# Optimization experiments

Measured on AMD Instinct MI355X. Metric: run time of the kernel, lower is better.

Reference implementation:

```python
import jax, jax.numpy as jnp
import numpy as np

N_ATOMS = 16384
APC = 64            # atoms per conformer
N_CONF = 256        # 64 mols * 4 confs
N_MOL = 64
DEG = 32
E = N_ATOMS * DEG
H = 128             # hidden_channels = num_filters = out_channels
G = 50              # num_gaussians
L = 6               # num_interactions
CUTOFF = 10.0
LOG2 = float(np.log(2.0))


def ssp(x):
    # ShiftedSoftplus: softplus(x) - log(2)
    return jax.nn.softplus(x) - LOG2


def setup_inputs() -> dict:
    key = jax.random.key(0)
    ks = jax.random.split(key, 24)
    rng = np.random.default_rng(0)

    z = jnp.asarray(rng.integers(1, 100, size=(N_ATOMS,)), dtype=jnp.int64 if jax.config.jax_enable_x64 else jnp.int32)
    # positions uniform in a 5A box -> all intra-conformer distances < cutoff
    pos = jax.random.uniform(ks[0], (N_ATOMS, 3), dtype=jnp.float32) * 5.0

    # within-conformer random edges, no self loops (radius_graph surrogate)
    i = np.repeat(np.arange(N_ATOMS), DEG)
    off = rng.integers(1, APC, size=E)
    j = (i // APC) * APC + (i % APC + off) % APC
    edge_index = jnp.asarray(np.stack([j, i]), dtype=jnp.int32)  # [2,E] (source, target)

    atom_to_conf = jnp.asarray(np.arange(N_ATOMS) // APC, dtype=jnp.int32)
    conf_to_mol = jnp.asarray(np.arange(N_CONF) // (N_CONF // N_MOL), dtype=jnp.int32)

    s = 0.05
    p = {
        'emb':     jax.random.normal(ks[1], (120, H), jnp.float32) * s,
        # per-interaction stacked params [L, ...]
        'mlp_w1':  jax.random.normal(ks[2], (L, G, H), jnp.float32) * s,
        'mlp_b1':  jnp.zeros((L, H), jnp.float32),
        'mlp_w2':  jax.random.normal(ks[3], (L, H, H), jnp.float32) * s,
        'mlp_b2':  jnp.zeros((L, H), jnp.float32),
        'cf_w1':   jax.random.normal(ks[4], (L, H, H), jnp.float32) * s,
        'cf_w2':   jax.random.normal(ks[5], (L, H, H), jnp.float32) * s,
        'cf_b2':   jnp.zeros((L, H), jnp.float32),
        'int_w':   jax.random.normal(ks[6], (L, H, H), jnp.float32) * s,
        'int_b':   jnp.zeros((L, H), jnp.float32),
        # readout head
        'out_w1':  jax.random.normal(ks[7], (H, H), jnp.float32) * s,
        'out_b1':  jnp.zeros((H,), jnp.float32),
        'out_w2':  jax.random.normal(ks[8], (H, H), jnp.float32) * s,
        'out_b2':  jnp.zeros((H,), jnp.float32),
        'head_w1': jax.random.normal(ks[9], (H, H // 2), jnp.float32) * s,
        'head_b1': jnp.zeros((H // 2,), jnp.float32),
        'head_w2': jax.random.normal(ks[10], (H // 2, 1), jnp.float32) * s,
        'head_b2': jnp.zeros((1,), jnp.float32),
    }
    return dict(z=z, pos=pos, edge_index=edge_index, atom_to_conf=atom_to_conf,
                conf_to_mol=conf_to_mol, **p)


def reference(z, pos, edge_index, atom_to_conf, conf_to_mol, emb,
              mlp_w1, mlp_b1, mlp_w2, mlp_b2, cf_w1, cf_w2, cf_b2,
              int_w, int_b, out_w1, out_b1, out_w2, out_b2,
              head_w1, head_b1, head_w2, head_b2):
    row, col = edge_index[0], edge_index[1]  # message from row, aggregated at col

    h = emb[z]                                             # [N,H]
    edge_weight = jnp.linalg.norm(pos[row] - pos[col], axis=-1)  # [E]

    # GaussianSmearing
    offset = jnp.linspace(0.0, CUTOFF, G)
    coeff = -0.5 / (offset[1] - offset[0]) ** 2
    edge_attr = jnp.exp(coeff * (edge_weight[:, None] - offset[None, :]) ** 2)  # [E,G]

    C = 0.5 * (jnp.cos(edge_weight * jnp.pi / CUTOFF) + 1.0)  # cosine cutoff [E]

    for l in range(L):
        # filter network on edge features, modulated by cutoff envelope
        Wf = ssp(edge_attr @ mlp_w1[l] + mlp_b1[l]) @ mlp_w2[l] + mlp_b2[l]
        Wf = Wf * C[:, None]                               # [E,H]
        xf = h @ cf_w1[l]                                  # lin1 (no bias) [N,H]
        msg = xf[row] * Wf                                 # gather * filter [E,H]
        agg = jax.ops.segment_sum(msg, col, num_segments=N_ATOMS)  # scatter-add [N,H]
        xc = agg @ cf_w2[l] + cf_b2[l]                     # lin2
        h = h + (ssp(xc) @ int_w[l] + int_b[l])            # act, lin, residual

    h = ssp(h @ out_w1 + out_b1)
    h = h @ out_w2 + out_b2                                # [N,H]

    conf_emb = jax.ops.segment_sum(h, atom_to_conf, num_segments=N_CONF)   # [C,H]
    mol_emb = jax.ops.segment_sum(conf_emb, conf_to_mol, num_segments=N_MOL)  # [M,H]

    out = (ssp(mol_emb @ head_w1 + head_b1) @ head_w2 + head_b2)[:, 0]  # [M]
    return out
```

## Files before the change

kernel.cpp:

```cpp
#include <hip/hip_runtime.h>
#include <math.h>

#define N_ATOMS 16384
#define APC 64
#define N_CONF 256
#define N_MOL 64
#define DEG 32
#define NEDGE (N_ATOMS * DEG)
#define H 128
#define G 50
#define NL 6
#define TP0 512
#define TPB 4096
#define CUTOFF 10.0f
#define WBLK 160
#define TBLK (NL * 256)

typedef __attribute__((ext_vector_type(8))) short short8_t;
typedef __attribute__((ext_vector_type(4))) float f32x4;
typedef __attribute__((ext_vector_type(2))) float f32x2;

__device__ __forceinline__ float ssp_f(float x) {
  float e = __expf(-fabsf(x));
  return fmaxf(x, 0.f) + __logf(1.f + e) - 0.69314718055994531f;
}
__device__ __forceinline__ unsigned short bf16_rne(float x) {
  unsigned u = __float_as_uint(x);
  unsigned r = u + 0x7FFF + ((u >> 16) & 1);
  return (unsigned short)(r >> 16);
}
__device__ __forceinline__ float bf16_to_f(unsigned short s) {
  return __uint_as_float(((unsigned)s) << 16);
}
__device__ __forceinline__ float bflo(unsigned u) { return __uint_as_float(u << 16); }
__device__ __forceinline__ float bfhi(unsigned u) { return __uint_as_float(u & 0xFFFF0000u); }

__global__ __launch_bounds__(256) void k_setup(
    const float* __restrict__ cf_w1, const float* __restrict__ cf_w2,
    const float* __restrict__ int_w, const float* __restrict__ out_w1,
    const float* __restrict__ out_w2, short* __restrict__ PW,
    const float* __restrict__ w1, const float* __restrict__ b1,
    const float* __restrict__ w2, const float* __restrict__ b2,
    unsigned short* __restrict__ Tb, int* __restrict__ cnt) {
  __shared__ float g2s[2][64];
  __shared__ float S2[2][128];
  __shared__ float OutS[4][132];
  const int b = blockIdx.x;
  const int tid = threadIdx.x;
  if (b == 0 && tid == 0) *cnt = 0;
  if (b < WBLK) {
    int e = b * 256 + tid;
    int g = e >> 11, t = e & 2047;
    int kb = t >> 9, rem = t & 511, nt = rem >> 6, lane = rem & 63;
    int quad = lane >> 4, ln2 = lane & 15;
    int kbase = kb * 32 + quad * 8;
    int n = nt * 16 + ln2;
    const float* src;
    if (g < 12) {
      int l = g >> 1;
      src = (g & 1) ? (int_w + l * 16384) : (cf_w2 + l * 16384);
    } else if (g < 18) {
      src = cf_w1 + (g - 12) * 16384;
    } else {
      src = (g == 18) ? out_w1 : out_w2;
    }
    short hv[8], lv[8];
    #pragma unroll
    for (int j = 0; j < 8; j++) {
      float x = src[(kbase + j) * H + n];
      unsigned short hb = bf16_rne(x);
      hv[j] = (short)hb;
      lv[j] = (short)bf16_rne(x - bf16_to_f(hb));
    }
    size_t base = (size_t)g * 32768 + (size_t)t * 8;
    *(short8_t*)&PW[base] = *(short8_t*)hv;
    *(short8_t*)&PW[base + 16384] = *(short8_t*)lv;
  } else {
    int bb = b - WBLK;
    const int l = bb >> 8, q = bb & 255;
    const int grp = tid >> 7, c = tid & 127;
    const int p_min =
        (int)((float)(q * 16) * ((float)(TP0 - 1) / (float)(TPB - 1)));
    const float gspace = CUTOFF / (float)(G - 1);
    const float coeff = -0.5f / (gspace * gspace);
    const float* W1 = w1 + l * G * H;
    const float* W2 = w2 + l * H * H;
    #pragma unroll 1
    for (int r = 0; r < 2; r++) {
      int pt = r * 2 + grp;
      int p = p_min + pt;
      if (p > TP0 - 1) p = TP0 - 1;
      float d = (float)p * (CUTOFF / (float)(TP0 - 1));
      if (c < G) {
        float x = d - (float)c * gspace;
        g2s[grp][c] = __expf(coeff * x * x);
      }
      __syncthreads();
      float s = b1[l * H + c];
      #pragma unroll 5
      for (int i = 0; i < G; i++) s += g2s[grp][i] * W1[i * H + c];
      S2[grp][c] = ssp_f(s);
      __syncthreads();
      float o = b2[l * H + c];
      #pragma unroll 8
      for (int j = 0; j < H; j++) o += S2[grp][j] * W2[j * H + c];
      float Cc = 0.5f * (__cosf(d * (3.14159265358979f / CUTOFF)) + 1.f);
      OutS[pt][c] = o * Cc;
      __syncthreads();
    }
    int p4o = tid >> 4, cg = tid & 15;
    int p4 = q * 16 + p4o;
    float u = (float)p4 * ((float)(TP0 - 1) / (float)(TPB - 1));
    int i = (int)u;
    if (i > TP0 - 2) i = TP0 - 2;
    float f = u - (float)i;
    int li = i - p_min;
    short8_t ov;
    #pragma unroll
    for (int j = 0; j < 4; j++) {
      float a0 = OutS[li][cg * 4 + j], a1 = OutS[li + 1][cg * 4 + j];
      ov[j] = (short)bf16_rne(a0 + f * (a1 - a0));
      float b0 = OutS[li][64 + cg * 4 + j], b1v = OutS[li + 1][64 + cg * 4 + j];
      ov[4 + j] = (short)bf16_rne(b0 + f * (b1v - b0));
    }
    *(short8_t*)&Tb[((size_t)l * TPB + p4) * H + cg * 8] = ov;
  }
}

#define MFMA(a, b, c) __builtin_amdgcn_mfma_f32_16x16x32_bf16((a), (b), (c), 0, 0, 0)

__device__ __forceinline__ void gemm_1x2(const short (*AH)[136], const short (*AL)[136],
                                         const short* __restrict__ pw,
                                         int rt, int ct2, int lane, int quad, int ln,
                                         f32x4 acc[2]) {
  #pragma unroll
  for (int kb = 0; kb < 4; kb++) {
    int ko = kb * 32 + quad * 8;
    int row = rt * 16 + ln;
    short8_t ah = *(const short8_t*)&AH[row][ko];
    short8_t al = *(const short8_t*)&AL[row][ko];
    #pragma unroll
    for (int ct = 0; ct < 2; ct++) {
      const short* pb = pw + ((size_t)(kb * 8 + ct2 * 2 + ct) * 64 + lane) * 8;
      short8_t bh = *(const short8_t*)pb;
      short8_t bl = *(const short8_t*)(pb + 16384);
      acc[ct] = MFMA(ah, bh, acc[ct]);
      acc[ct] = MFMA(ah, bl, acc[ct]);
      acc[ct] = MFMA(al, bh, acc[ct]);
    }
  }
}

__global__ __launch_bounds__(1024, 1) void k_mega(
    const int* __restrict__ z, const float* __restrict__ emb,
    const float* __restrict__ pos, const int* __restrict__ esrc,
    const unsigned short* __restrict__ Tb,
    const short* __restrict__ PW, const float* __restrict__ cf_b2,
    const float* __restrict__ int_b, const float* __restrict__ out_b1,
    const float* __restrict__ out_b2, float* __restrict__ ce,
    const float* __restrict__ hw1, const float* __restrict__ hb1,
    const float* __restrict__ hw2, const float* __restrict__ hb2,
    int* __restrict__ cnt, float* __restrict__ outp) {
  __shared__ float xs[64][132];
  __shared__ __align__(16) short hH[64][136], hL[64][136];
  __shared__ __align__(16) short tH[64][136], tL[64][136];
  __shared__ __align__(16) short S1H[64][136], S1L[64][136];
  __shared__ int pks[2048];
  __shared__ float ps[4][128];
  __shared__ int is_last;
  const int conf = blockIdx.x;
  const int tid = threadIdx.x;
  const int lane = tid & 63, w = tid >> 6;
  const int quad = lane >> 4, ln = lane & 15;
  const int rt = w & 3, ct2 = w >> 2;
  const int eg = lane >> 4, c0 = (lane & 15) * 4;

  float* posl = &xs[0][0];
  if (tid < 192) posl[tid] = pos[conf * 192 + tid];

  {
    int r = tid >> 4, cb = (tid & 15) * 8;
    const float* src = emb + (size_t)z[conf * 64 + r] * H + cb;
    float4 v0 = *(const float4*)src, v1 = *(const float4*)(src + 4);
    float vv[8] = {v0.x, v0.y, v0.z, v0.w, v1.x, v1.y, v1.z, v1.w};
    short hv[8], lv[8];
    #pragma unroll
    for (int u = 0; u < 8; u++) {
      unsigned short hb = bf16_rne(vv[u]);
      hv[u] = (short)hb;
      lv[u] = (short)bf16_rne(vv[u] - bf16_to_f(hb));
    }
    *(short8_t*)&hH[r][cb] = *(short8_t*)hv;
    *(short8_t*)&hL[r][cb] = *(short8_t*)lv;
  }
  __syncthreads();

  #pragma unroll
  for (int e0 = 0; e0 < 2; e0++) {
    int e = e0 * 1024 + tid;
    int s = esrc[conf * 2048 + e] & (APC - 1);
    int t = e >> 5;
    float dx = posl[s * 3 + 0] - posl[t * 3 + 0];
    float dy = posl[s * 3 + 1] - posl[t * 3 + 1];
    float dz = posl[s * 3 + 2] - posl[t * 3 + 2];
    float d = sqrtf(dx * dx + dy * dy + dz * dz);
    int i = (int)(d * ((float)(TPB - 1) / CUTOFF) + 0.5f);
    if (i > TPB - 1) i = TPB - 1;
    if (i < 0) i = 0;
    pks[e] = (i << 8) | (s << 20);
  }
  __syncthreads();

  {
    f32x4 acc[2] = {{0.f, 0.f, 0.f, 0.f}, {0.f, 0.f, 0.f, 0.f}};
    gemm_1x2(hH, hL, PW + (size_t)12 * 32768, rt, ct2, lane, quad, ln, acc);
    #pragma unroll
    for (int ct = 0; ct < 2; ct++) {
      int col = (ct2 * 2 + ct) * 16 + ln;
      #pragma unroll
      for (int reg = 0; reg < 4; reg++)
        xs[rt * 16 + quad * 4 + reg][col] = acc[ct][reg];
    }
  }
  __syncthreads();

  for (int l = 0; l < NL; l++) {
    const char* Tlb = (const char*)(Tb + (size_t)l * TPB * H) + ln * 16;
    #pragma unroll 1
    for (int aa = 0; aa < 4; aa++) {
      int a2 = w * 4 + aa;
      int ms[8];
      uint4 tvv[8];
      #pragma unroll
      for (int it = 0; it < 8; it++) {
        ms[it] = pks[a2 * DEG + it * 4 + eg];
        tvv[it] = *(const uint4*)(Tlb + (ms[it] & 0xFFFFF));
      }
      f32x2 ac0 = {0.f, 0.f}, ac1 = {0.f, 0.f}, ac2 = {0.f, 0.f}, ac3 = {0.f, 0.f};
      #pragma unroll
      for (int it = 0; it < 8; it++) {
        int sl = ms[it] >> 20;
        const float* xr = &xs[sl][c0];
        float4 x0 = *(const float4*)xr;
        float4 x1 = *(const float4*)(xr + 64);
        uint4 tv = tvv[it];
        ac0 = __builtin_elementwise_fma((f32x2){bflo(tv.x), bfhi(tv.x)},
                                        (f32x2){x0.x, x0.y}, ac0);
        ac1 = __builtin_elementwise_fma((f32x2){bflo(tv.y), bfhi(tv.y)},
                                        (f32x2){x0.z, x0.w}, ac1);
        ac2 = __builtin_elementwise_fma((f32x2){bflo(tv.z), bfhi(tv.z)},
                                        (f32x2){x1.x, x1.y}, ac2);
        ac3 = __builtin_elementwise_fma((f32x2){bflo(tv.w), bfhi(tv.w)},
                                        (f32x2){x1.z, x1.w}, ac3);
      }
      float accs[8] = {ac0.x, ac0.y, ac1.x, ac1.y, ac2.x, ac2.y, ac3.x, ac3.y};
      #pragma unroll
      for (int j = 0; j < 8; j++) {
        accs[j] += __shfl_xor(accs[j], 16);
        accs[j] += __shfl_xor(accs[j], 32);
      }
      float va = eg == 0 ? accs[0] : eg == 1 ? accs[2] : eg == 2 ? accs[4] : accs[6];
      float vb = eg == 0 ? accs[1] : eg == 1 ? accs[3] : eg == 2 ? accs[5] : accs[7];
      unsigned short ha = bf16_rne(va), hb = bf16_rne(vb);
      unsigned short la = bf16_rne(va - bf16_to_f(ha));
      unsigned short lb = bf16_rne(vb - bf16_to_f(hb));
      int cw = (eg >> 1) * 64 + c0 + (eg & 1) * 2;
      *(short2*)&S1H[a2][cw] = make_short2((short)ha, (short)hb);
      *(short2*)&S1L[a2][cw] = make_short2((short)la, (short)lb);
    }
    __syncthreads();
    {
      f32x4 acc[2] = {{0.f, 0.f, 0.f, 0.f}, {0.f, 0.f, 0.f, 0.f}};
      gemm_1x2(S1H, S1L, PW + (size_t)(2 * l) * 32768, rt, ct2, lane, quad, ln, acc);
      #pragma unroll
      for (int ct = 0; ct < 2; ct++) {
        int col = (ct2 * 2 + ct) * 16 + ln;
        float bb = cf_b2[l * H + col];
        #pragma unroll
        for (int reg = 0; reg < 4; reg++) {
          int row = rt * 16 + quad * 4 + reg;
          float v = ssp_f(acc[ct][reg] + bb);
          unsigned short hb = bf16_rne(v);
          tH[row][col] = (short)hb;
          tL[row][col] = (short)bf16_rne(v - bf16_to_f(hb));
        }
      }
    }
    __syncthreads();
    {
      f32x4 acc[2] = {{0.f, 0.f, 0.f, 0.f}, {0.f, 0.f, 0.f, 0.f}};
      gemm_1x2(tH, tL, PW + (size_t)(2 * l + 1) * 32768, rt, ct2, lane, quad, ln, acc);
      #pragma unroll
      for (int ct = 0; ct < 2; ct++) {
        int col = (ct2 * 2 + ct) * 16 + ln;
        float bb = int_b[l * H + col];
        #pragma unroll
        for (int reg = 0; reg < 4; reg++) {
          int row = rt * 16 + quad * 4 + reg;
          float hv = bf16_to_f((unsigned short)hH[row][col]) +
                     bf16_to_f((unsigned short)hL[row][col]);
          float v = acc[ct][reg] + bb + hv;
          unsigned short hb = bf16_rne(v);
          hH[row][col] = (short)hb;
          hL[row][col] = (short)bf16_rne(v - bf16_to_f(hb));
        }
      }
    }
    __syncthreads();
    if (l < NL - 1) {
      f32x4 acc[2] = {{0.f, 0.f, 0.f, 0.f}, {0.f, 0.f, 0.f, 0.f}};
      gemm_1x2(hH, hL, PW + (size_t)(13 + l) * 32768, rt, ct2, lane, quad, ln, acc);
      #pragma unroll
      for (int ct = 0; ct < 2; ct++) {
        int col = (ct2 * 2 + ct) * 16 + ln;
        #pragma unroll
        for (int reg = 0; reg < 4; reg++)
          xs[rt * 16 + quad * 4 + reg][col] = acc[ct][reg];
      }
      __syncthreads();
    }
  }

  {
    f32x4 acc[2] = {{0.f, 0.f, 0.f, 0.f}, {0.f, 0.f, 0.f, 0.f}};
    gemm_1x2(hH, hL, PW + (size_t)18 * 32768, rt, ct2, lane, quad, ln, acc);
    #pragma unroll
    for (int ct = 0; ct < 2; ct++) {
      int col = (ct2 * 2 + ct) * 16 + ln;
      float bb = out_b1[col];
      #pragma unroll
      for (int reg = 0; reg < 4; reg++) {
        int row = rt * 16 + quad * 4 + reg;
        float v = ssp_f(acc[ct][reg] + bb);
        unsigned short hb = bf16_rne(v);
        tH[row][col] = (short)hb;
        tL[row][col] = (short)bf16_rne(v - bf16_to_f(hb));
      }
    }
  }
  __syncthreads();
  {
    f32x4 acc[2] = {{0.f, 0.f, 0.f, 0.f}, {0.f, 0.f, 0.f, 0.f}};
    gemm_1x2(tH, tL, PW + (size_t)19 * 32768, rt, ct2, lane, quad, ln, acc);
    #pragma unroll
    for (int ct = 0; ct < 2; ct++) {
      int col = (ct2 * 2 + ct) * 16 + ln;
      float s = acc[ct][0] + acc[ct][1] + acc[ct][2] + acc[ct][3];
      s += __shfl_xor(s, 16);
      s += __shfl_xor(s, 32);
      if (quad == 0) ps[rt][col] = s;
    }
  }
  __syncthreads();
  if (tid < 128) {
    float v = ps[0][tid] + ps[1][tid] + ps[2][tid] + ps[3][tid] +
              64.f * out_b2[tid];
    __hip_atomic_store(&ce[conf * 128 + tid], v, __ATOMIC_RELAXED,
                       __HIP_MEMORY_SCOPE_AGENT);
  }
  __syncthreads();
  if (tid == 0) {
    __threadfence();
    int old = __hip_atomic_fetch_add(cnt, 1, __ATOMIC_ACQ_REL,
                                     __HIP_MEMORY_SCOPE_AGENT);
    is_last = (old == N_CONF - 1) ? 1 : 0;
  }
  __syncthreads();
  if (is_last) {
    __threadfence();
    float* mol = &xs[0][0];
    for (int t = tid; t < N_MOL * 128; t += 1024) {
      int m = t >> 7, c = t & 127;
      const float* b = ce + (size_t)(m * 4) * 128;
      float s = __hip_atomic_load(&b[c], __ATOMIC_RELAXED, __HIP_MEMORY_SCOPE_AGENT) +
                __hip_atomic_load(&b[128 + c], __ATOMIC_RELAXED, __HIP_MEMORY_SCOPE_AGENT) +
                __hip_atomic_load(&b[256 + c], __ATOMIC_RELAXED, __HIP_MEMORY_SCOPE_AGENT) +
                __hip_atomic_load(&b[384 + c], __ATOMIC_RELAXED, __HIP_MEMORY_SCOPE_AGENT);
      mol[t] = s;
    }
    __syncthreads();
    float* q = (float*)&S1H[0][0];
    for (int t = tid; t < N_MOL * 64; t += 1024) {
      int m = t >> 6, j = t & 63;
      float qq = hb1[j];
      #pragma unroll 8
      for (int c = 0; c < H; c++) qq += mol[m * 128 + c] * hw1[c * 64 + j];
      q[t] = ssp_f(qq);
    }
    __syncthreads();
    if (tid < N_MOL) {
      float o = hb2[0];
      #pragma unroll 8
      for (int j = 0; j < 64; j++) o += q[tid * 64 + j] * hw2[j];
      outp[tid] = o;
    }
  }
}

extern "C" void kernel_launch(void* const* d_in, const int* in_sizes, int n_in,
                              void* d_out, int out_size, void* d_ws, size_t ws_size,
                              hipStream_t stream) {
  const int*   z       = (const int*)d_in[0];
  const float* pos     = (const float*)d_in[1];
  const int*   eidx    = (const int*)d_in[2];
  const float* emb     = (const float*)d_in[5];
  const float* mlp_w1  = (const float*)d_in[6];
  const float* mlp_b1  = (const float*)d_in[7];
  const float* mlp_w2  = (const float*)d_in[8];
  const float* mlp_b2  = (const float*)d_in[9];
  const float* cf_w1   = (const float*)d_in[10];
  const float* cf_w2   = (const float*)d_in[11];
  const float* cf_b2   = (const float*)d_in[12];
  const float* int_w   = (const float*)d_in[13];
  const float* int_b   = (const float*)d_in[14];
  const float* out_w1  = (const float*)d_in[15];
  const float* out_b1  = (const float*)d_in[16];
  const float* out_w2  = (const float*)d_in[17];
  const float* out_b2  = (const float*)d_in[18];
  const float* head_w1 = (const float*)d_in[19];
  const float* head_b1 = (const float*)d_in[20];
  const float* head_w2 = (const float*)d_in[21];
  const float* head_b2 = (const float*)d_in[22];

  char* ws = (char*)d_ws;
  unsigned short* Tb = (unsigned short*)ws;
  short* PW  = (short*)(ws + (size_t)NL * TPB * H * 2);
  float* ce  = (float*)((char*)PW + (size_t)20 * 32768 * 2);
  int*   cnt = (int*)((char*)ce + (size_t)N_CONF * H * 4);

  k_setup<<<WBLK + TBLK, 256, 0, stream>>>(cf_w1, cf_w2, int_w, out_w1, out_w2,
                                           PW, mlp_w1, mlp_b1, mlp_w2, mlp_b2,
                                           Tb, cnt);

  k_mega<<<N_CONF, 1024, 0, stream>>>(z, emb, pos, eidx, Tb, PW, cf_b2, int_b,
                                      out_b1, out_b2, ce,
                                      head_w1, head_b1, head_w2, head_b2,
                                      cnt, (float*)d_out);
}
```

Baseline: 262.9 us.

## Retile warp GEMMs to 32x16 tiles, prefetch gather loads, keep residual in registers

Result: slower. 359.5 us (+36.8%).

```diff
diff --git a/kernel.cpp b/kernel.cpp
--- a/kernel.cpp
+++ b/kernel.cpp
@@ -129,24 +129,28 @@
 
 #define MFMA(a, b, c) __builtin_amdgcn_mfma_f32_16x16x32_bf16((a), (b), (c), 0, 0, 0)
 
-__device__ __forceinline__ void gemm_1x2(const short (*AH)[136], const short (*AL)[136],
+__device__ __forceinline__ void gemm_rt2(const short (*AH)[140], const short (*AL)[140],
                                          const short* __restrict__ pw,
-                                         int rt, int ct2, int lane, int quad, int ln,
+                                         int rt2, int nt, int lane, int quad, int ln,
                                          f32x4 acc[2]) {
+  short8_t bh[4], bl[4];
+  #pragma unroll
+  for (int kb = 0; kb < 4; kb++) {
+    const short* pb = pw + ((size_t)(kb * 8 + nt) * 64 + lane) * 8;
+    bh[kb] = *(const short8_t*)pb;
+    bl[kb] = *(const short8_t*)(pb + 16384);
+  }
   #pragma unroll
   for (int kb = 0; kb < 4; kb++) {
     int ko = kb * 32 + quad * 8;
-    int row = rt * 16 + ln;
-    short8_t ah = *(const short8_t*)&AH[row][ko];
-    short8_t al = *(const short8_t*)&AL[row][ko];
-    #pragma unroll
-    for (int ct = 0; ct < 2; ct++) {
-      const short* pb = pw + ((size_t)(kb * 8 + ct2 * 2 + ct) * 64 + lane) * 8;
-      short8_t bh = *(const short8_t*)pb;
-      short8_t bl = *(const short8_t*)(pb + 16384);
-      acc[ct] = MFMA(ah, bh, acc[ct]);
-      acc[ct] = MFMA(ah, bl, acc[ct]);
-      acc[ct] = MFMA(al, bh, acc[ct]);
+    #pragma unroll
+    for (int rtt = 0; rtt < 2; rtt++) {
+      int row = rt2 * 32 + rtt * 16 + ln;
+      short8_t ah = *(const short8_t*)&AH[row][ko];
+      short8_t al = *(const short8_t*)&AL[row][ko];
+      acc[rtt] = MFMA(ah, bh[kb], acc[rtt]);
+      acc[rtt] = MFMA(ah, bl[kb], acc[rtt]);
+      acc[rtt] = MFMA(al, bh[kb], acc[rtt]);
     }
   }
 }
@@ -162,18 +166,19 @@
     const float* __restrict__ hw2, const float* __restrict__ hb2,
     int* __restrict__ cnt, float* __restrict__ outp) {
   __shared__ float xs[64][132];
-  __shared__ __align__(16) short hH[64][136], hL[64][136];
-  __shared__ __align__(16) short tH[64][136], tL[64][136];
-  __shared__ __align__(16) short S1H[64][136], S1L[64][136];
+  __shared__ __align__(16) short hH[64][140], hL[64][140];
+  __shared__ __align__(16) short tH[64][140], tL[64][140];
+  __shared__ __align__(16) short S1H[64][140], S1L[64][140];
   __shared__ int pks[2048];
-  __shared__ float ps[4][128];
+  __shared__ float ps[2][128];
   __shared__ int is_last;
   const int conf = blockIdx.x;
   const int tid = threadIdx.x;
   const int lane = tid & 63, w = tid >> 6;
   const int quad = lane >> 4, ln = lane & 15;
-  const int rt = w & 3, ct2 = w >> 2;
+  const int rt2 = w & 1, nt = w >> 1;
   const int eg = lane >> 4, c0 = (lane & 15) * 4;
+  const int col = nt * 16 + ln;
 
   float* posl = &xs[0][0];
   if (tid < 192) posl[tid] = pos[conf * 192 + tid];
@@ -194,6 +199,16 @@
     *(short8_t*)&hL[r][cb] = *(short8_t*)lv;
   }
   __syncthreads();
+
+  f32x4 hreg[2];
+  #pragma unroll
+  for (int rtt = 0; rtt < 2; rtt++)
+    #pragma unroll
+    for (int reg = 0; reg < 4; reg++) {
+      int row = rt2 * 32 + rtt * 16 + quad * 4 + reg;
+      hreg[rtt][reg] = bf16_to_f((unsigned short)hH[row][col]) +
+                       bf16_to_f((unsigned short)hL[row][col]);
+    }
 
   #pragma unroll
   for (int e0 = 0; e0 < 2; e0++) {
@@ -213,28 +228,35 @@
 
   {
     f32x4 acc[2] = {{0.f, 0.f, 0.f, 0.f}, {0.f, 0.f, 0.f, 0.f}};
-    gemm_1x2(hH, hL, PW + (size_t)12 * 32768, rt, ct2, lane, quad, ln, acc);
-    #pragma unroll
-    for (int ct = 0; ct < 2; ct++) {
-      int col = (ct2 * 2 + ct) * 16 + ln;
+    gemm_rt2(hH, hL, PW + (size_t)12 * 32768, rt2, nt, lane, quad, ln, acc);
+    #pragma unroll
+    for (int rtt = 0; rtt < 2; rtt++)
       #pragma unroll
       for (int reg = 0; reg < 4; reg++)
-        xs[rt * 16 + quad * 4 + reg][col] = acc[ct][reg];
-    }
+        xs[rt2 * 32 + rtt * 16 + quad * 4 + reg][col] = acc[rtt][reg];
   }
   __syncthreads();
 
   for (int l = 0; l < NL; l++) {
     const char* Tlb = (const char*)(Tb + (size_t)l * TPB * H) + ln * 16;
+    int ms[8];
+    uint4 tvv[8];
+    #pragma unroll
+    for (int it = 0; it < 8; it++) {
+      ms[it] = pks[(w * 4) * DEG + it * 4 + eg];
+      tvv[it] = *(const uint4*)(Tlb + (ms[it] & 0xFFFFF));
+    }
     #pragma unroll 1
     for (int aa = 0; aa < 4; aa++) {
       int a2 = w * 4 + aa;
-      int ms[8];
-      uint4 tvv[8];
-      #pragma unroll
-      for (int it = 0; it < 8; it++) {
-        ms[it] = pks[a2 * DEG + it * 4 + eg];
-        tvv[it] = *(const uint4*)(Tlb + (ms[it] & 0xFFFFF));
+      int msn[8];
+      uint4 tvn[8];
+      if (aa < 3) {
+        #pragma unroll
+        for (int it = 0; it < 8; it++) {
+          msn[it] = pks[(a2 + 1) * DEG + it * 4 + eg];
+          tvn[it] = *(const uint4*)(Tlb + (msn[it] & 0xFFFFF));
+        }
       }
       f32x2 ac0 = {0.f, 0.f}, ac1 = {0.f, 0.f}, ac2 = {0.f, 0.f}, ac3 = {0.f, 0.f};
       #pragma unroll
@@ -267,94 +289,88 @@
       int cw = (eg >> 1) * 64 + c0 + (eg & 1) * 2;
       *(short2*)&S1H[a2][cw] = make_short2((short)ha, (short)hb);
       *(short2*)&S1L[a2][cw] = make_short2((short)la, (short)lb);
+      if (aa < 3) {
+        #pragma unroll
+        for (int it = 0; it < 8; it++) {
+          ms[it] = msn[it];
+          tvv[it] = tvn[it];
+        }
+      }
     }
     __syncthreads();
     {
       f32x4 acc[2] = {{0.f, 0.f, 0.f, 0.f}, {0.f, 0.f, 0.f, 0.f}};
-      gemm_1x2(S1H, S1L, PW + (size_t)(2 * l) * 32768, rt, ct2, lane, quad, ln, acc);
-      #pragma unroll
-      for (int ct = 0; ct < 2; ct++) {
-        int col = (ct2 * 2 + ct) * 16 + ln;
-        float bb = cf_b2[l * H + col];
+      gemm_rt2(S1H, S1L, PW + (size_t)(2 * l) * 32768, rt2, nt, lane, quad, ln, acc);
+      float bb = cf_b2[l * H + col];
+      #pragma unroll
+      for (int rtt = 0; rtt < 2; rtt++)
         #pragma unroll
         for (int reg = 0; reg < 4; reg++) {
-          int row = rt * 16 + quad * 4 + reg;
-          float v = ssp_f(acc[ct][reg] + bb);
+          int row = rt2 * 32 + rtt * 16 + quad * 4 + reg;
+          float v = ssp_f(acc[rtt][reg] + bb);
           unsigned short hb = bf16_rne(v);
           tH[row][col] = (short)hb;
           tL[row][col] = (short)bf16_rne(v - bf16_to_f(hb));
         }
-      }
     }
     __syncthreads();
     {
       f32x4 acc[2] = {{0.f, 0.f, 0.f, 0.f}, {0.f, 0.f, 0.f, 0.f}};
-      gemm_1x2(tH, tL, PW + (size_t)(2 * l + 1) * 32768, rt, ct2, lane, quad, ln, acc);
-      #pragma unroll
-      for (int ct = 0; ct < 2; ct++) {
-        int col = (ct2 * 2 + ct) * 16 + ln;
-        float bb = int_b[l * H + col];
+      gemm_rt2(tH, tL, PW + (size_t)(2 * l + 1) * 32768, rt2, nt, lane, quad, ln, acc);
+      float bb = int_b[l * H + col];
+      #pragma unroll
+      for (int rtt = 0; rtt < 2; rtt++)
         #pragma unroll
         for (int reg = 0; reg < 4; reg++) {
-          int row = rt * 16 + quad * 4 + reg;
-          float hv = bf16_to_f((unsigned short)hH[row][col]) +
-                     bf16_to_f((unsigned short)hL[row][col]);
-          float v = acc[ct][reg] + bb + hv;
+          int row = rt2 * 32 + rtt * 16 + quad * 4 + reg;
+          float v = acc[rtt][reg] + bb + hreg[rtt][reg];
+          hreg[rtt][reg] = v;
           unsigned short hb = bf16_rne(v);
           hH[row][col] = (short)hb;
           hL[row][col] = (short)bf16_rne(v - bf16_to_f(hb));
         }
-      }
     }
     __syncthreads();
     if (l < NL - 1) {
       f32x4 acc[2] = {{0.f, 0.f, 0.f, 0.f}, {0.f, 0.f, 0.f, 0.f}};
-      gemm_1x2(hH, hL, PW + (size_t)(13 + l) * 32768, rt, ct2, lane, quad, ln, acc);
-      #pragma unroll
-      for (int ct = 0; ct < 2; ct++) {
-        int col = (ct2 * 2 + ct) * 16 + ln;
+      gemm_rt2(hH, hL, PW + (size_t)(13 + l) * 32768, rt2, nt, lane, quad, ln, acc);
+      #pragma unroll
+      for (int rtt = 0; rtt < 2; rtt++)
         #pragma unroll
         for (int reg = 0; reg < 4; reg++)
-          xs[rt * 16 + quad * 4 + reg][col] = acc[ct][reg];
-      }
+          xs[rt2 * 32 + rtt * 16 + quad * 4 + reg][col] = acc[rtt][reg];
       __syncthreads();
     }
   }
 
   {
     f32x4 acc[2] = {{0.f, 0.f, 0.f, 0.f}, {0.f, 0.f, 0.f, 0.f}};
-    gemm_1x2(hH, hL, PW + (size_t)18 * 32768, rt, ct2, lane, quad, ln, acc);
-    #pragma unroll
-    for (int ct = 0; ct < 2; ct++) {
-      int col = (ct2 * 2 + ct) * 16 + ln;
-      float bb = out_b1[col];
+    gemm_rt2(hH, hL, PW + (size_t)18 * 32768, rt2, nt, lane, quad, ln, acc);
+    float bb = out_b1[col];
+    #pragma unroll
+    for (int rtt = 0; rtt < 2; rtt++)
       #pragma unroll
       for (int reg = 0; reg < 4; reg++) {
-        int row = rt * 16 + quad * 4 + reg;
-        float v = ssp_f(acc[ct][reg] + bb);
+        int row = rt2 * 32 + rtt * 16 + quad * 4 + reg;
+        float v = ssp_f(acc[rtt][reg] + bb);
         unsigned short hb = bf16_rne(v);
         tH[row][col] = (short)hb;
         tL[row][col] = (short)bf16_rne(v - bf16_to_f(hb));
       }
-    }
   }
   __syncthreads();
   {
     f32x4 acc[2] = {{0.f, 0.f, 0.f, 0.f}, {0.f, 0.f, 0.f, 0.f}};
-    gemm_1x2(tH, tL, PW + (size_t)19 * 32768, rt, ct2, lane, quad, ln, acc);
-    #pragma unroll
-    for (int ct = 0; ct < 2; ct++) {
-      int col = (ct2 * 2 + ct) * 16 + ln;
-      float s = acc[ct][0] + acc[ct][1] + acc[ct][2] + acc[ct][3];
-      s += __shfl_xor(s, 16);
-      s += __shfl_xor(s, 32);
-      if (quad == 0) ps[rt][col] = s;
-    }
+    gemm_rt2(tH, tL, PW + (size_t)19 * 32768, rt2, nt, lane, quad, ln, acc);
+    float s = acc[0][0] + acc[0][1] + acc[0][2] + acc[0][3] +
+              acc[1][0] + acc[1][1] + acc[1][2] + acc[1][3];
+    s += __shfl_xor(s, 16);
+    s += __shfl_xor(s, 32);
+    if (quad == 0) ps[rt2][col] = s;
   }
   __syncthreads();
   if (tid < 128) {
-    float v = ps[0][tid] + ps[1][tid] + ps[2][tid] + ps[3][tid] +
-              64.f * out_b2[tid];
+    float v = ps[0][tid] + ps[1][tid] + 64.f * out_b2[tid];
     __hip_atomic_store(&ce[conf * 128 + tid], v, __ATOMIC_RELAXED,
                        __HIP_MEMORY_SCOPE_AGENT);
   }
```
